# Optimization experiments

Measured on AMD Instinct MI355X. Metric: run time of the kernel, lower is better.

Reference implementation:

```python
import jax, jax.numpy as jnp
import numpy as np

NUM_EMBEDDINGS = 1024
EMBEDDING_DIM = 256
COMMITMENT_COST = 0.25


def setup_inputs() -> dict:
    key = jax.random.key(0)
    k1, k2 = jax.random.split(key)
    inputs = jax.random.normal(k1, (64, 32, 32, EMBEDDING_DIM), dtype=jnp.float32)
    embed = jax.random.normal(k2, (NUM_EMBEDDINGS, EMBEDDING_DIM), dtype=jnp.float32)
    return {"inputs": inputs, "embed": embed}


def reference(inputs, embed):
    # Eval-mode forward (no EMA buffer mutation), use_ema=True loss branch.
    input_shape = inputs.shape
    flat = inputs.reshape(-1, EMBEDDING_DIM)  # [N, d]
    distances = (
        jnp.sum(flat * flat, axis=1, keepdims=True)
        + jnp.sum(embed * embed, axis=1)
        - 2.0 * jnp.matmul(flat, embed.T)
    )
    encoding_indices = jnp.argmin(distances, axis=1)  # [N]
    # Gather codebook rows (equivalent to one-hot @ embed)
    quantized = embed[encoding_indices].reshape(input_shape)
    # use_ema branch: loss = commitment * mse(stop_grad(quantized), inputs)
    e_latent_loss = jnp.mean((jax.lax.stop_gradient(quantized) - inputs) ** 2)
    loss = COMMITMENT_COST * e_latent_loss
    # Straight-through estimator
    quantized_st = inputs + jax.lax.stop_gradient(quantized - inputs)
    # Perplexity from code usage histogram (== mean of one-hot encodings)
    n_tokens = flat.shape[0]
    counts = jax.ops.segment_sum(
        jnp.ones((n_tokens,), dtype=jnp.float32), encoding_indices,
        num_segments=NUM_EMBEDDINGS)
    avg_probs = counts / n_tokens
    perplexity = jnp.exp(-jnp.sum(avg_probs * jnp.log(avg_probs + 1e-10)))
    return quantized_st, loss, perplexity, encoding_indices
```

## Files before the change

kernel.cpp:

```cpp
#include <hip/hip_runtime.h>

#define NTOK 65536
#define DIM 256
#define KC 1024
#define EPS 0.08f

typedef __attribute__((ext_vector_type(8))) _Float16 f16x8;
typedef __attribute__((ext_vector_type(8))) unsigned short u16x8;
typedef __attribute__((ext_vector_type(4))) float f32x4;

static __device__ __forceinline__ unsigned short f16bits(float f) {
  _Float16 h = (_Float16)f;
  return __builtin_bit_cast(unsigned short, h);
}

__global__ __launch_bounds__(256) void vq_prep_e(const float* __restrict__ e,
                                                 unsigned short* __restrict__ eg,
                                                 float* __restrict__ esq,
                                                 int* __restrict__ hist,
                                                 int* __restrict__ fixCount) {
  const int gid = blockIdx.x * 256 + threadIdx.x;
  const int t = gid >> 5;
  const int o = gid & 31;
  const float4 v0 = *reinterpret_cast<const float4*>(&e[t * DIM + o * 8]);
  const float4 v1 = *reinterpret_cast<const float4*>(&e[t * DIM + o * 8 + 4]);
  u16x8 u;
  u[0] = f16bits(v0.x); u[1] = f16bits(v0.y); u[2] = f16bits(v0.z); u[3] = f16bits(v0.w);
  u[4] = f16bits(v1.x); u[5] = f16bits(v1.y); u[6] = f16bits(v1.z); u[7] = f16bits(v1.w);
  const int ct = t >> 7, nj = (t >> 4) & 7, col = t & 15;
  const int s = o >> 2, kq = o & 3;
  char* dst = (char*)eg + ((ct * 64 + s * 8 + nj) << 10) + ((kq * 16 + col) << 4);
  *reinterpret_cast<u16x8*>(dst) = u;
  float p = v0.x * v0.x + v0.y * v0.y + v0.z * v0.z + v0.w * v0.w +
            v1.x * v1.x + v1.y * v1.y + v1.z * v1.z + v1.w * v1.w;
#pragma unroll
  for (int m = 16; m > 0; m >>= 1) p += __shfl_xor(p, m, 64);
  if (o == 0) esq[t] = p;
  if (blockIdx.x < 4) hist[blockIdx.x * 256 + threadIdx.x] = 0;
  if (gid == 0) *fixCount = 0;
}

__global__ __launch_bounds__(64, 4) void vq_argmin(
    const float* __restrict__ x, const unsigned short* __restrict__ eg,
    const float* __restrict__ esq, const float* __restrict__ e,
    float* __restrict__ outIdxF, float* __restrict__ outQ,
    float* __restrict__ bestDist, float* __restrict__ xsq,
    int* __restrict__ hist, int* __restrict__ fixCount,
    unsigned int* __restrict__ fixList) {
  const int lane = threadIdx.x;
  const int col = lane & 15, kq = lane >> 4;
  const int tw = blockIdx.x * 16;

  f16x8 a[8];
  float sq = 0.f;
#pragma unroll
  for (int s = 0; s < 8; ++s) {
    const float* xp = &x[(tw + col) * DIM + s * 32 + kq * 8];
    const float4 v0 = *reinterpret_cast<const float4*>(xp);
    const float4 v1 = *reinterpret_cast<const float4*>(xp + 4);
    a[s][0] = (_Float16)v0.x; a[s][1] = (_Float16)v0.y;
    a[s][2] = (_Float16)v0.z; a[s][3] = (_Float16)v0.w;
    a[s][4] = (_Float16)v1.x; a[s][5] = (_Float16)v1.y;
    a[s][6] = (_Float16)v1.z; a[s][7] = (_Float16)v1.w;
    sq += v0.x * v0.x + v0.y * v0.y + v0.z * v0.z + v0.w * v0.w +
          v1.x * v1.x + v1.y * v1.y + v1.z * v1.z + v1.w * v1.w;
  }
  sq += __shfl_xor(sq, 16, 64);
  sq += __shfl_xor(sq, 32, 64);
  if (lane < 16) xsq[tw + lane] = sq;

  float v1_[4], v2_[4], v3_[4];
  int i1_[4], i2_[4];
#pragma unroll
  for (int r = 0; r < 4; ++r) {
    v1_[r] = 3.4e38f; v2_[r] = 3.4e38f; v3_[r] = 3.4e38f;
    i1_[r] = 0; i2_[r] = 0;
  }

  for (int ct = 0; ct < 8; ++ct) {
    const char* ebase = (const char*)eg + ct * 65536;
    f32x4 acc[8];
#pragma unroll
    for (int nj = 0; nj < 8; ++nj) acc[nj] = (f32x4){0.f, 0.f, 0.f, 0.f};

#pragma unroll
    for (int s = 0; s < 8; ++s) {
      f16x8 b[8];
#pragma unroll
      for (int nj = 0; nj < 8; ++nj)
        b[nj] = *reinterpret_cast<const f16x8*>(
            ebase + ((s * 8 + nj) << 10) + (lane << 4));
#pragma unroll
      for (int nj = 0; nj < 8; ++nj)
        acc[nj] = __builtin_amdgcn_mfma_f32_16x16x32_f16(a[s], b[nj], acc[nj], 0, 0, 0);
    }

#pragma unroll
    for (int nj = 0; nj < 8; ++nj) {
      const int code = ct * 128 + nj * 16 + col;
      const float sqv = esq[code];
#pragma unroll
      for (int r = 0; r < 4; ++r) {
        const float d = fmaf(-2.f, acc[nj][r], sqv);
        if (d < v1_[r]) {
          v3_[r] = v2_[r]; v2_[r] = v1_[r]; i2_[r] = i1_[r];
          v1_[r] = d; i1_[r] = code;
        } else if (d < v2_[r]) {
          v3_[r] = v2_[r]; v2_[r] = d; i2_[r] = code;
        } else if (d < v3_[r]) {
          v3_[r] = d;
        }
      }
    }
  }

#pragma unroll
  for (int r = 0; r < 4; ++r) {
    float mv1 = v1_[r], mv2 = v2_[r], mv3 = v3_[r];
    int mi1 = i1_[r], mi2 = i2_[r];
#pragma unroll
    for (int m = 1; m <= 8; m <<= 1) {
      const float ov1 = __shfl_xor(mv1, m, 64);
      const float ov2 = __shfl_xor(mv2, m, 64);
      const float ov3 = __shfl_xor(mv3, m, 64);
      const int oi1 = __shfl_xor(mi1, m, 64);
      const int oi2 = __shfl_xor(mi2, m, 64);
      const bool oW = (ov1 < mv1) || (ov1 == mv1 && oi1 < mi1);
      const float wv1 = oW ? ov1 : mv1, wv2 = oW ? ov2 : mv2, wv3 = oW ? ov3 : mv3;
      const int wi1 = oW ? oi1 : mi1, wi2 = oW ? oi2 : mi2;
      const float lv1 = oW ? mv1 : ov1, lv2 = oW ? mv2 : ov2;
      const int li1 = oW ? mi1 : oi1;
      const bool w2 = (wv2 < lv1) || (wv2 == lv1 && wi2 < li1);
      mv1 = wv1; mi1 = wi1;
      mv2 = w2 ? wv2 : lv1;
      mi2 = w2 ? wi2 : li1;
      mv3 = w2 ? fminf(wv3, lv1) : fminf(wv2, lv2);
    }
    if (col == 0) {
      const int t = tw + kq * 4 + r;
      outIdxF[t] = (float)mi1;
      bestDist[t] = mv1;
      atomicAdd(&hist[mi1], 1);
      if (mv2 - mv1 < EPS) {
        const unsigned full = (mv3 - mv1 < EPS) ? 0x80000000u : 0u;
        const int p = atomicAdd(fixCount, 1);
        fixList[p * 2] = (unsigned)t | full;
        fixList[p * 2 + 1] = (unsigned)mi2;
      }
    }
    i1_[r] = mi1;
  }

#pragma unroll
  for (int i = 0; i < 16; ++i) {
    const int id = __shfl(i1_[i & 3], (i >> 2) * 16, 64);
    const float4 q = reinterpret_cast<const float4*>(&e[id * DIM])[lane];
    reinterpret_cast<float4*>(&outQ[(tw + i) * DIM])[lane] = q;
  }
}

__global__ __launch_bounds__(256) void vq_fixup(
    const float* __restrict__ x, const float* __restrict__ e,
    const int* __restrict__ fixCount, const unsigned int* __restrict__ fixList,
    float* __restrict__ outIdxF, float* __restrict__ outQ,
    float* __restrict__ bestDist, int* __restrict__ hist) {
  const int n = *fixCount;
  const int tid = threadIdx.x;
  __shared__ float xrow[256];
  __shared__ float rv[4];
  __shared__ int ri[4];
  __shared__ int sOld, sFi;
  for (int it = blockIdx.x; it < n; it += gridDim.x) {
    const unsigned e0 = fixList[it * 2];
    const int t = (int)(e0 & 0x3FFFFFFFu);
    const bool full = (e0 >> 31) != 0u;
    if (!full) {
      if (tid < 64) {
        const int i1 = (int)outIdxF[t];
        const int i2 = (int)fixList[it * 2 + 1];
        const float4 xv = reinterpret_cast<const float4*>(&x[t * DIM])[tid];
        const float4 e1 = reinterpret_cast<const float4*>(&e[i1 * DIM])[tid];
        const float4 e2 = reinterpret_cast<const float4*>(&e[i2 * DIM])[tid];
        float d1 = (xv.x - e1.x) * (xv.x - e1.x) + (xv.y - e1.y) * (xv.y - e1.y) +
                   (xv.z - e1.z) * (xv.z - e1.z) + (xv.w - e1.w) * (xv.w - e1.w);
        float d2 = (xv.x - e2.x) * (xv.x - e2.x) + (xv.y - e2.y) * (xv.y - e2.y) +
                   (xv.z - e2.z) * (xv.z - e2.z) + (xv.w - e2.w) * (xv.w - e2.w);
#pragma unroll
        for (int m = 32; m > 0; m >>= 1) {
          d1 += __shfl_xor(d1, m, 64);
          d2 += __shfl_xor(d2, m, 64);
        }
        const bool swap2 = (d2 < d1) || (d2 == d1 && i2 < i1);
        const int wIdx = swap2 ? i2 : i1;
        const float wD = swap2 ? d2 : d1;
        if (tid == 0) {
          bestDist[t] = wD;
          if (wIdx != i1) {
            atomicSub(&hist[i1], 1);
            atomicAdd(&hist[wIdx], 1);
            outIdxF[t] = (float)wIdx;
          }
        }
        if (swap2) {
          const float4 q = reinterpret_cast<const float4*>(&e[wIdx * DIM])[tid];
          reinterpret_cast<float4*>(&outQ[t * DIM])[tid] = q;
        }
      }
    } else {
      __syncthreads();
      if (tid < 64) ((float4*)xrow)[tid] = ((const float4*)&x[t * DIM])[tid];
      __syncthreads();
      float bv = 3.4e38f; int bi = 0;
      for (int c = tid; c < KC; c += 256) {
        float s = 0.f;
#pragma unroll
        for (int d = 0; d < DIM; d += 4) {
          const float4 ev = *(const float4*)&e[c * DIM + d];
          const float d0 = xrow[d] - ev.x, d1 = xrow[d + 1] - ev.y;
          const float d2 = xrow[d + 2] - ev.z, d3 = xrow[d + 3] - ev.w;
          s += d0 * d0 + d1 * d1 + d2 * d2 + d3 * d3;
        }
        if (s < bv) { bv = s; bi = c; }
      }
#pragma unroll
      for (int m = 1; m <= 32; m <<= 1) {
        const float ob = __shfl_xor(bv, m, 64);
        const int oi = __shfl_xor(bi, m, 64);
        if (ob < bv || (ob == bv && oi < bi)) { bv = ob; bi = oi; }
      }
      const int lane = tid & 63, wv = tid >> 6;
      if (lane == 0) { rv[wv] = bv; ri[wv] = bi; }
      __syncthreads();
      if (tid == 0) {
        float fb = rv[0]; int fi = ri[0];
        for (int k = 1; k < 4; ++k)
          if (rv[k] < fb || (rv[k] == fb && ri[k] < fi)) { fb = rv[k]; fi = ri[k]; }
        sOld = (int)outIdxF[t];
        sFi = fi;
        bestDist[t] = fb;
        if (fi != sOld) {
          atomicSub(&hist[sOld], 1);
          atomicAdd(&hist[fi], 1);
          outIdxF[t] = (float)fi;
        }
      }
      __syncthreads();
      if (sFi != sOld) outQ[t * DIM + tid] = e[sFi * DIM + tid];
      __syncthreads();
    }
  }
}

__global__ __launch_bounds__(1024) void vq_final(
    const int* __restrict__ hist, const float* __restrict__ xsq,
    const float* __restrict__ bestDist, float* __restrict__ outLoss,
    float* __restrict__ outPerp) {
  const int tid = threadIdx.x;
  float ls = 0.f;
  for (int i = 0; i < 64; ++i) {
    const int t = tid + i * 1024;
    ls += xsq[t] + bestDist[t];
  }
  const float p = (float)hist[tid] * (1.f / 65536.f);
  float ent = p * logf(p + 1e-10f);
#pragma unroll
  for (int o = 32; o > 0; o >>= 1) {
    ls += __shfl_down(ls, o, 64);
    ent += __shfl_down(ent, o, 64);
  }
  __shared__ float lbuf[16], ebuf[16];
  const int lane = tid & 63, wv = tid >> 6;
  if (lane == 0) { lbuf[wv] = ls; ebuf[wv] = ent; }
  __syncthreads();
  if (tid == 0) {
    float L = 0.f, E = 0.f;
    for (int i = 0; i < 16; ++i) { L += lbuf[i]; E += ebuf[i]; }
    *outLoss = 0.25f * (L / 16777216.f);
    *outPerp = expf(-E);
  }
}

extern "C" void kernel_launch(void* const* d_in, const int* in_sizes, int n_in,
                              void* d_out, int out_size, void* d_ws, size_t ws_size,
                              hipStream_t stream) {
  const float* x = (const float*)d_in[0];
  const float* e = (const float*)d_in[1];
  float* out = (float*)d_out;
  float* outQ = out;
  float* outLoss = out + 16777216;
  float* outPerp = out + 16777217;
  float* outIdxF = out + 16777218;

  char* ws = (char*)d_ws;
  int*   hist     = (int*)ws;
  float* esq      = (float*)(ws + 4096);
  float* xsq      = (float*)(ws + 8192);
  float* bestDist = (float*)(ws + 270336);
  int*   fixCount = (int*)(ws + 532480);
  unsigned int* fixList = (unsigned int*)(ws + 532496);
  unsigned short* e_f16 = (unsigned short*)(ws + 1056784);

  vq_prep_e<<<128, 256, 0, stream>>>(e, e_f16, esq, hist, fixCount);
  vq_argmin<<<NTOK / 16, 64, 0, stream>>>(x, e_f16, esq, e, outIdxF, outQ,
                                          bestDist, xsq, hist, fixCount, fixList);
  vq_fixup<<<256, 256, 0, stream>>>(x, e, fixCount, fixList, outIdxF, outQ,
                                    bestDist, hist);
  vq_final<<<1, 1024, 0, stream>>>(hist, xsq, bestDist, outLoss, outPerp);
}
```

Measured before the change: 189.8 us.

## Double-buffer codebook fragment loads and pack four waves per argmin block

The argmin kernel now software-pipelines the f16 codebook loads with two register buffers, so the next k-slice, including the first slice of the next code tile, is fetched while MFMAs run on the current one. Blocks grow from one wave to four waves covering 64 tokens, with launch bounds changed to 256 threads and 3 blocks per CU. The aim is to hide global/L2 load latency behind matrix work. In exchange it doubles the B-fragment register footprint, which may push register use up and lower occupancy.

```diff
diff --git a/kernel.cpp b/kernel.cpp
--- a/kernel.cpp
+++ b/kernel.cpp
@@ -40,16 +40,16 @@
   if (gid == 0) *fixCount = 0;
 }
 
-__global__ __launch_bounds__(64, 4) void vq_argmin(
+__global__ __launch_bounds__(256, 3) void vq_argmin(
     const float* __restrict__ x, const unsigned short* __restrict__ eg,
     const float* __restrict__ esq, const float* __restrict__ e,
     float* __restrict__ outIdxF, float* __restrict__ outQ,
     float* __restrict__ bestDist, float* __restrict__ xsq,
     int* __restrict__ hist, int* __restrict__ fixCount,
     unsigned int* __restrict__ fixList) {
-  const int lane = threadIdx.x;
+  const int lane = threadIdx.x & 63, w = threadIdx.x >> 6;
   const int col = lane & 15, kq = lane >> 4;
-  const int tw = blockIdx.x * 16;
+  const int tw = blockIdx.x * 64 + w * 16;
 
   f16x8 a[8];
   float sq = 0.f;
@@ -69,6 +69,18 @@
   sq += __shfl_xor(sq, 32, 64);
   if (lane < 16) xsq[tw + lane] = sq;
 
+  auto LD8 = [&](f16x8 (&buf)[8], const char* eb, int s) {
+#pragma unroll
+    for (int nj = 0; nj < 8; ++nj)
+      buf[nj] = *reinterpret_cast<const f16x8*>(
+          eb + ((s * 8 + nj) << 10) + (lane << 4));
+  };
+  auto MF8 = [&](const f16x8& av, f16x8 (&buf)[8], f32x4 (&acc)[8]) {
+#pragma unroll
+    for (int nj = 0; nj < 8; ++nj)
+      acc[nj] = __builtin_amdgcn_mfma_f32_16x16x32_f16(av, buf[nj], acc[nj], 0, 0, 0);
+  };
+
   float v1_[4], v2_[4], v3_[4];
   int i1_[4], i2_[4];
 #pragma unroll
@@ -77,23 +89,24 @@
     i1_[r] = 0; i2_[r] = 0;
   }
 
+  f16x8 bA[8], bB[8];
+  LD8(bA, (const char*)eg, 0);
+
   for (int ct = 0; ct < 8; ++ct) {
-    const char* ebase = (const char*)eg + ct * 65536;
+    const char* eb = (const char*)eg + ct * 65536;
     f32x4 acc[8];
 #pragma unroll
     for (int nj = 0; nj < 8; ++nj) acc[nj] = (f32x4){0.f, 0.f, 0.f, 0.f};
 
-#pragma unroll
-    for (int s = 0; s < 8; ++s) {
-      f16x8 b[8];
-#pragma unroll
-      for (int nj = 0; nj < 8; ++nj)
-        b[nj] = *reinterpret_cast<const f16x8*>(
-            ebase + ((s * 8 + nj) << 10) + (lane << 4));
-#pragma unroll
-      for (int nj = 0; nj < 8; ++nj)
-        acc[nj] = __builtin_amdgcn_mfma_f32_16x16x32_f16(a[s], b[nj], acc[nj], 0, 0, 0);
-    }
+    LD8(bB, eb, 1); MF8(a[0], bA, acc);
+    LD8(bA, eb, 2); MF8(a[1], bB, acc);
+    LD8(bB, eb, 3); MF8(a[2], bA, acc);
+    LD8(bA, eb, 4); MF8(a[3], bB, acc);
+    LD8(bB, eb, 5); MF8(a[4], bA, acc);
+    LD8(bA, eb, 6); MF8(a[5], bB, acc);
+    LD8(bB, eb, 7); MF8(a[6], bA, acc);
+    if (ct < 7) LD8(bA, eb + 65536, 0);
+    MF8(a[7], bB, acc);
 
 #pragma unroll
     for (int nj = 0; nj < 8; ++nj) {
@@ -301,8 +314,8 @@
   unsigned short* e_f16 = (unsigned short*)(ws + 1056784);
 
   vq_prep_e<<<128, 256, 0, stream>>>(e, e_f16, esq, hist, fixCount);
-  vq_argmin<<<NTOK / 16, 64, 0, stream>>>(x, e_f16, esq, e, outIdxF, outQ,
-                                          bestDist, xsq, hist, fixCount, fixList);
+  vq_argmin<<<NTOK / 64, 256, 0, stream>>>(x, e_f16, esq, e, outIdxF, outQ,
+                                           bestDist, xsq, hist, fixCount, fixList);
   vq_fixup<<<256, 256, 0, stream>>>(x, e, fixCount, fixList, outIdxF, outQ,
                                     bestDist, hist);
   vq_final<<<1, 1024, 0, stream>>>(hist, xsq, bestDist, outLoss, outPerp);
```

Result: slower. 208.9 us (+10.0%).

## Pipeline codebook loads with inline asm and double tokens per wave

Applied to the files above, without the earlier changes.

Each wave now handles 32 tokens (two 16-row A tiles) instead of 16, so every codebook fragment loaded feeds twice as many MFMAs, and blocks grow to four waves. The codebook layout is regrouped into 64-code chunks, streamed through a four-stage register ring with inline-asm global loads and explicit vmcnt waits plus sched barriers, so loads overlap the MFMAs. This targets codebook load bandwidth and exposed latency, at the cost of higher register pressure (two waves per SIMD bound) and fragile hand-counted waitcnt logic.

```diff
diff --git a/kernel.cpp b/kernel.cpp
--- a/kernel.cpp
+++ b/kernel.cpp
@@ -13,6 +13,12 @@
   _Float16 h = (_Float16)f;
   return __builtin_bit_cast(unsigned short, h);
 }
+
+#define VWAIT(n) asm volatile("s_waitcnt vmcnt(" #n ")" ::: "memory")
+#define SB() __builtin_amdgcn_sched_barrier(0)
+#define GLDX4(dst, p, off) \
+  asm volatile("global_load_dwordx4 %0, %1, off offset:" #off \
+               : "=v"(dst) : "v"(p) : "memory")
 
 __global__ __launch_bounds__(256) void vq_prep_e(const float* __restrict__ e,
                                                  unsigned short* __restrict__ eg,
@@ -27,9 +33,9 @@
   u16x8 u;
   u[0] = f16bits(v0.x); u[1] = f16bits(v0.y); u[2] = f16bits(v0.z); u[3] = f16bits(v0.w);
   u[4] = f16bits(v1.x); u[5] = f16bits(v1.y); u[6] = f16bits(v1.z); u[7] = f16bits(v1.w);
-  const int ct = t >> 7, nj = (t >> 4) & 7, col = t & 15;
+  const int ctk = t >> 6, njj = (t >> 4) & 3, col = t & 15;
   const int s = o >> 2, kq = o & 3;
-  char* dst = (char*)eg + ((ct * 64 + s * 8 + nj) << 10) + ((kq * 16 + col) << 4);
+  char* dst = (char*)eg + ((ctk * 32 + s * 4 + njj) << 10) + ((kq * 16 + col) << 4);
   *reinterpret_cast<u16x8*>(dst) = u;
   float p = v0.x * v0.x + v0.y * v0.y + v0.z * v0.z + v0.w * v0.w +
             v1.x * v1.x + v1.y * v1.y + v1.z * v1.z + v1.w * v1.w;
@@ -40,120 +46,185 @@
   if (gid == 0) *fixCount = 0;
 }
 
-__global__ __launch_bounds__(64, 4) void vq_argmin(
+__global__ __launch_bounds__(256, 2) void vq_argmin(
     const float* __restrict__ x, const unsigned short* __restrict__ eg,
     const float* __restrict__ esq, const float* __restrict__ e,
     float* __restrict__ outIdxF, float* __restrict__ outQ,
     float* __restrict__ bestDist, float* __restrict__ xsq,
     int* __restrict__ hist, int* __restrict__ fixCount,
     unsigned int* __restrict__ fixList) {
-  const int lane = threadIdx.x;
+  const int lane = threadIdx.x & 63, w = threadIdx.x >> 6;
   const int col = lane & 15, kq = lane >> 4;
-  const int tw = blockIdx.x * 16;
-
-  f16x8 a[8];
-  float sq = 0.f;
-#pragma unroll
-  for (int s = 0; s < 8; ++s) {
-    const float* xp = &x[(tw + col) * DIM + s * 32 + kq * 8];
-    const float4 v0 = *reinterpret_cast<const float4*>(xp);
-    const float4 v1 = *reinterpret_cast<const float4*>(xp + 4);
-    a[s][0] = (_Float16)v0.x; a[s][1] = (_Float16)v0.y;
-    a[s][2] = (_Float16)v0.z; a[s][3] = (_Float16)v0.w;
-    a[s][4] = (_Float16)v1.x; a[s][5] = (_Float16)v1.y;
-    a[s][6] = (_Float16)v1.z; a[s][7] = (_Float16)v1.w;
-    sq += v0.x * v0.x + v0.y * v0.y + v0.z * v0.z + v0.w * v0.w +
-          v1.x * v1.x + v1.y * v1.y + v1.z * v1.z + v1.w * v1.w;
-  }
-  sq += __shfl_xor(sq, 16, 64);
-  sq += __shfl_xor(sq, 32, 64);
-  if (lane < 16) xsq[tw + lane] = sq;
-
-  float v1_[4], v2_[4], v3_[4];
-  int i1_[4], i2_[4];
-#pragma unroll
-  for (int r = 0; r < 4; ++r) {
-    v1_[r] = 3.4e38f; v2_[r] = 3.4e38f; v3_[r] = 3.4e38f;
-    i1_[r] = 0; i2_[r] = 0;
-  }
-
-  for (int ct = 0; ct < 8; ++ct) {
-    const char* ebase = (const char*)eg + ct * 65536;
-    f32x4 acc[8];
-#pragma unroll
-    for (int nj = 0; nj < 8; ++nj) acc[nj] = (f32x4){0.f, 0.f, 0.f, 0.f};
-
+  const int tw = blockIdx.x * 128 + w * 32;
+
+  f16x8 a[2][8];
+  float sqm[2] = {0.f, 0.f};
+#pragma unroll
+  for (int mi = 0; mi < 2; ++mi) {
 #pragma unroll
     for (int s = 0; s < 8; ++s) {
-      f16x8 b[8];
-#pragma unroll
-      for (int nj = 0; nj < 8; ++nj)
-        b[nj] = *reinterpret_cast<const f16x8*>(
-            ebase + ((s * 8 + nj) << 10) + (lane << 4));
-#pragma unroll
-      for (int nj = 0; nj < 8; ++nj)
-        acc[nj] = __builtin_amdgcn_mfma_f32_16x16x32_f16(a[s], b[nj], acc[nj], 0, 0, 0);
-    }
-
-#pragma unroll
-    for (int nj = 0; nj < 8; ++nj) {
-      const int code = ct * 128 + nj * 16 + col;
-      const float sqv = esq[code];
-#pragma unroll
-      for (int r = 0; r < 4; ++r) {
-        const float d = fmaf(-2.f, acc[nj][r], sqv);
-        if (d < v1_[r]) {
-          v3_[r] = v2_[r]; v2_[r] = v1_[r]; i2_[r] = i1_[r];
-          v1_[r] = d; i1_[r] = code;
-        } else if (d < v2_[r]) {
-          v3_[r] = v2_[r]; v2_[r] = d; i2_[r] = code;
-        } else if (d < v3_[r]) {
-          v3_[r] = d;
-        }
-      }
-    }
-  }
-
-#pragma unroll
-  for (int r = 0; r < 4; ++r) {
-    float mv1 = v1_[r], mv2 = v2_[r], mv3 = v3_[r];
-    int mi1 = i1_[r], mi2 = i2_[r];
-#pragma unroll
-    for (int m = 1; m <= 8; m <<= 1) {
-      const float ov1 = __shfl_xor(mv1, m, 64);
-      const float ov2 = __shfl_xor(mv2, m, 64);
-      const float ov3 = __shfl_xor(mv3, m, 64);
-      const int oi1 = __shfl_xor(mi1, m, 64);
-      const int oi2 = __shfl_xor(mi2, m, 64);
-      const bool oW = (ov1 < mv1) || (ov1 == mv1 && oi1 < mi1);
-      const float wv1 = oW ? ov1 : mv1, wv2 = oW ? ov2 : mv2, wv3 = oW ? ov3 : mv3;
-      const int wi1 = oW ? oi1 : mi1, wi2 = oW ? oi2 : mi2;
-      const float lv1 = oW ? mv1 : ov1, lv2 = oW ? mv2 : ov2;
-      const int li1 = oW ? mi1 : oi1;
-      const bool w2 = (wv2 < lv1) || (wv2 == lv1 && wi2 < li1);
-      mv1 = wv1; mi1 = wi1;
-      mv2 = w2 ? wv2 : lv1;
-      mi2 = w2 ? wi2 : li1;
-      mv3 = w2 ? fminf(wv3, lv1) : fminf(wv2, lv2);
-    }
-    if (col == 0) {
-      const int t = tw + kq * 4 + r;
-      outIdxF[t] = (float)mi1;
-      bestDist[t] = mv1;
-      atomicAdd(&hist[mi1], 1);
-      if (mv2 - mv1 < EPS) {
-        const unsigned full = (mv3 - mv1 < EPS) ? 0x80000000u : 0u;
-        const int p = atomicAdd(fixCount, 1);
-        fixList[p * 2] = (unsigned)t | full;
-        fixList[p * 2 + 1] = (unsigned)mi2;
-      }
-    }
-    i1_[r] = mi1;
-  }
-
-#pragma unroll
-  for (int i = 0; i < 16; ++i) {
-    const int id = __shfl(i1_[i & 3], (i >> 2) * 16, 64);
+      const float* xp = &x[(tw + mi * 16 + col) * DIM + s * 32 + kq * 8];
+      const float4 v0 = *reinterpret_cast<const float4*>(xp);
+      const float4 v1 = *reinterpret_cast<const float4*>(xp + 4);
+      a[mi][s][0] = (_Float16)v0.x; a[mi][s][1] = (_Float16)v0.y;
+      a[mi][s][2] = (_Float16)v0.z; a[mi][s][3] = (_Float16)v0.w;
+      a[mi][s][4] = (_Float16)v1.x; a[mi][s][5] = (_Float16)v1.y;
+      a[mi][s][6] = (_Float16)v1.z; a[mi][s][7] = (_Float16)v1.w;
+      sqm[mi] += v0.x * v0.x + v0.y * v0.y + v0.z * v0.z + v0.w * v0.w +
+                 v1.x * v1.x + v1.y * v1.y + v1.z * v1.z + v1.w * v1.w;
+    }
+  }
+#pragma unroll
+  for (int mi = 0; mi < 2; ++mi) {
+    sqm[mi] += __shfl_xor(sqm[mi], 16, 64);
+    sqm[mi] += __shfl_xor(sqm[mi], 32, 64);
+  }
+  if (lane < 16) {
+    xsq[tw + lane] = sqm[0];
+    xsq[tw + 16 + lane] = sqm[1];
+  }
+
+  float v1_[2][4], v2_[2][4], v3_[2][4];
+  int i1_[2][4], i2_[2][4];
+#pragma unroll
+  for (int mi = 0; mi < 2; ++mi)
+#pragma unroll
+    for (int r = 0; r < 4; ++r) {
+      v1_[mi][r] = 3.4e38f; v2_[mi][r] = 3.4e38f; v3_[mi][r] = 3.4e38f;
+      i1_[mi][r] = 0; i2_[mi][r] = 0;
+    }
+
+  f32x4 acc[2][4];
+  f16x8 B[4][4];
+  const char* p = (const char*)eg + lane * 16;
+
+  VWAIT(0);
+  SB();
+#pragma unroll
+  for (int g = 0; g < 4; ++g) {
+    GLDX4(B[g][0], p, 0); GLDX4(B[g][1], p, 1024);
+    GLDX4(B[g][2], p, 2048); GLDX4(B[g][3], p, 3072);
+    p += 4096;
+  }
+
+#define STEP_BODY(S, BUF)                                                     \
+  do {                                                                        \
+    acc[0][0] = __builtin_amdgcn_mfma_f32_16x16x32_f16(a[0][(S)], BUF[0], acc[0][0], 0, 0, 0); \
+    acc[0][1] = __builtin_amdgcn_mfma_f32_16x16x32_f16(a[0][(S)], BUF[1], acc[0][1], 0, 0, 0); \
+    acc[0][2] = __builtin_amdgcn_mfma_f32_16x16x32_f16(a[0][(S)], BUF[2], acc[0][2], 0, 0, 0); \
+    acc[0][3] = __builtin_amdgcn_mfma_f32_16x16x32_f16(a[0][(S)], BUF[3], acc[0][3], 0, 0, 0); \
+    acc[1][0] = __builtin_amdgcn_mfma_f32_16x16x32_f16(a[1][(S)], BUF[0], acc[1][0], 0, 0, 0); \
+    acc[1][1] = __builtin_amdgcn_mfma_f32_16x16x32_f16(a[1][(S)], BUF[1], acc[1][1], 0, 0, 0); \
+    acc[1][2] = __builtin_amdgcn_mfma_f32_16x16x32_f16(a[1][(S)], BUF[2], acc[1][2], 0, 0, 0); \
+    acc[1][3] = __builtin_amdgcn_mfma_f32_16x16x32_f16(a[1][(S)], BUF[3], acc[1][3], 0, 0, 0); \
+  } while (0)
+
+#define ISSUE(BUF)                                                 \
+  do {                                                             \
+    GLDX4(BUF[0], p, 0); GLDX4(BUF[1], p, 1024);                   \
+    GLDX4(BUF[2], p, 2048); GLDX4(BUF[3], p, 3072);                \
+    p += 4096;                                                     \
+  } while (0)
+
+#define EPILOGUE(CTK)                                                         \
+  do {                                                                        \
+    const float* pe = &esq[(CTK) * 64 + col];                                 \
+    _Pragma("unroll") for (int njj = 0; njj < 4; ++njj) {                     \
+      const int code = (CTK) * 64 + njj * 16 + col;                           \
+      const float sqv = pe[njj * 16];                                         \
+      _Pragma("unroll") for (int mi = 0; mi < 2; ++mi)                        \
+      _Pragma("unroll") for (int r = 0; r < 4; ++r) {                         \
+        const float d = fmaf(-2.f, acc[mi][njj][r], sqv);                     \
+        if (d < v1_[mi][r]) {                                                 \
+          v3_[mi][r] = v2_[mi][r]; v2_[mi][r] = v1_[mi][r];                   \
+          i2_[mi][r] = i1_[mi][r];                                            \
+          v1_[mi][r] = d; i1_[mi][r] = code;                                  \
+        } else if (d < v2_[mi][r]) {                                          \
+          v3_[mi][r] = v2_[mi][r]; v2_[mi][r] = d; i2_[mi][r] = code;         \
+        } else if (d < v3_[mi][r]) {                                          \
+          v3_[mi][r] = d;                                                     \
+        }                                                                     \
+      }                                                                       \
+    }                                                                         \
+  } while (0)
+
+  for (int ctk = 0; ctk < 15; ++ctk) {
+#pragma unroll
+    for (int mi = 0; mi < 2; ++mi)
+#pragma unroll
+      for (int nj = 0; nj < 4; ++nj) acc[mi][nj] = (f32x4){0.f, 0.f, 0.f, 0.f};
+#pragma unroll
+    for (int s = 0; s < 8; ++s) {
+      VWAIT(12);
+      SB();
+      if ((s & 3) == 0) { STEP_BODY(s, B[0]); ISSUE(B[0]); }
+      else if ((s & 3) == 1) { STEP_BODY(s, B[1]); ISSUE(B[1]); }
+      else if ((s & 3) == 2) { STEP_BODY(s, B[2]); ISSUE(B[2]); }
+      else { STEP_BODY(s, B[3]); ISSUE(B[3]); }
+    }
+    EPILOGUE(ctk);
+  }
+  {
+#pragma unroll
+    for (int mi = 0; mi < 2; ++mi)
+#pragma unroll
+      for (int nj = 0; nj < 4; ++nj) acc[mi][nj] = (f32x4){0.f, 0.f, 0.f, 0.f};
+    VWAIT(12); SB(); STEP_BODY(0, B[0]); ISSUE(B[0]);
+    VWAIT(12); SB(); STEP_BODY(1, B[1]); ISSUE(B[1]);
+    VWAIT(12); SB(); STEP_BODY(2, B[2]); ISSUE(B[2]);
+    VWAIT(12); SB(); STEP_BODY(3, B[3]); ISSUE(B[3]);
+    VWAIT(12); SB(); STEP_BODY(4, B[0]);
+    VWAIT(8);  SB(); STEP_BODY(5, B[1]);
+    VWAIT(4);  SB(); STEP_BODY(6, B[2]);
+    VWAIT(0);  SB(); STEP_BODY(7, B[3]);
+    EPILOGUE(15);
+  }
+#undef STEP_BODY
+#undef ISSUE
+#undef EPILOGUE
+
+#pragma unroll
+  for (int mi = 0; mi < 2; ++mi)
+#pragma unroll
+    for (int r = 0; r < 4; ++r) {
+      float mv1 = v1_[mi][r], mv2 = v2_[mi][r], mv3 = v3_[mi][r];
+      int mi1 = i1_[mi][r], mi2 = i2_[mi][r];
+#pragma unroll
+      for (int m = 1; m <= 8; m <<= 1) {
+        const float ov1 = __shfl_xor(mv1, m, 64);
+        const float ov2 = __shfl_xor(mv2, m, 64);
+        const float ov3 = __shfl_xor(mv3, m, 64);
+        const int oi1 = __shfl_xor(mi1, m, 64);
+        const int oi2 = __shfl_xor(mi2, m, 64);
+        const bool oW = (ov1 < mv1) || (ov1 == mv1 && oi1 < mi1);
+        const float wv1 = oW ? ov1 : mv1, wv2 = oW ? ov2 : mv2, wv3 = oW ? ov3 : mv3;
+        const int wi1 = oW ? oi1 : mi1, wi2 = oW ? oi2 : mi2;
+        const float lv1 = oW ? mv1 : ov1, lv2 = oW ? mv2 : ov2;
+        const int li1 = oW ? mi1 : oi1;
+        const bool w2 = (wv2 < lv1) || (wv2 == lv1 && wi2 < li1);
+        mv1 = wv1; mi1 = wi1;
+        mv2 = w2 ? wv2 : lv1;
+        mi2 = w2 ? wi2 : li1;
+        mv3 = w2 ? fminf(wv3, lv1) : fminf(wv2, lv2);
+      }
+      if (col == 0) {
+        const int t = tw + mi * 16 + kq * 4 + r;
+        outIdxF[t] = (float)mi1;
+        bestDist[t] = mv1;
+        atomicAdd(&hist[mi1], 1);
+        if (mv2 - mv1 < EPS) {
+          const unsigned full = (mv3 - mv1 < EPS) ? 0x80000000u : 0u;
+          const int pp = atomicAdd(fixCount, 1);
+          fixList[pp * 2] = (unsigned)t | full;
+          fixList[pp * 2 + 1] = (unsigned)mi2;
+        }
+      }
+      i1_[mi][r] = mi1;
+    }
+
+#pragma unroll
+  for (int i = 0; i < 32; ++i) {
+    const int id = __shfl(i1_[i >> 4][i & 3], ((i >> 2) & 3) * 16, 64);
     const float4 q = reinterpret_cast<const float4*>(&e[id * DIM])[lane];
     reinterpret_cast<float4*>(&outQ[(tw + i) * DIM])[lane] = q;
   }
@@ -301,8 +372,8 @@
   unsigned short* e_f16 = (unsigned short*)(ws + 1056784);
 
   vq_prep_e<<<128, 256, 0, stream>>>(e, e_f16, esq, hist, fixCount);
-  vq_argmin<<<NTOK / 16, 64, 0, stream>>>(x, e_f16, esq, e, outIdxF, outQ,
-                                          bestDist, xsq, hist, fixCount, fixList);
+  vq_argmin<<<NTOK / 128, 256, 0, stream>>>(x, e_f16, esq, e, outIdxF, outQ,
+                                            bestDist, xsq, hist, fixCount, fixList);
   vq_fixup<<<256, 256, 0, stream>>>(x, e, fixCount, fixList, outIdxF, outQ,
                                     bestDist, hist);
   vq_final<<<1, 1024, 0, stream>>>(hist, xsq, bestDist, outLoss, outPerp);
```

After: 164.9 us. -13.2%, faster.

## Swap MFMA operand roles: keep codebook slices in registers, stream pre-converted tokens

Applied to the files above, without the earlier changes.

Adds a prep kernel that converts inputs to f16 in an MFMA-friendly tiled layout and computes row norms. The argmin kernel now holds a 32-code slice of the codebook in registers per wave and streams token tiles through it. Each code partition writes per-token top-2 partial results to scratch space carved from the output buffer. A new finish kernel reduces the 32 partials per token and builds the fixup list, and a separate gather kernel writes the quantized rows. This removes the repeated full-codebook reload per 16-token wave, at the cost of extra kernels and roughly 1 GB of extra global traffic for the f16 copy and partial results, plus more atomics.

```diff
diff --git a/kernel.cpp b/kernel.cpp
--- a/kernel.cpp
+++ b/kernel.cpp
@@ -27,9 +27,9 @@
   u16x8 u;
   u[0] = f16bits(v0.x); u[1] = f16bits(v0.y); u[2] = f16bits(v0.z); u[3] = f16bits(v0.w);
   u[4] = f16bits(v1.x); u[5] = f16bits(v1.y); u[6] = f16bits(v1.z); u[7] = f16bits(v1.w);
-  const int ct = t >> 7, nj = (t >> 4) & 7, col = t & 15;
+  const int ctk = t >> 6, njj = (t >> 4) & 3, col = t & 15;
   const int s = o >> 2, kq = o & 3;
-  char* dst = (char*)eg + ((ct * 64 + s * 8 + nj) << 10) + ((kq * 16 + col) << 4);
+  char* dst = (char*)eg + ((ctk * 32 + s * 4 + njj) << 10) + ((kq * 16 + col) << 4);
   *reinterpret_cast<u16x8*>(dst) = u;
   float p = v0.x * v0.x + v0.y * v0.y + v0.z * v0.z + v0.w * v0.w +
             v1.x * v1.x + v1.y * v1.y + v1.z * v1.z + v1.w * v1.w;
@@ -40,122 +40,158 @@
   if (gid == 0) *fixCount = 0;
 }
 
-__global__ __launch_bounds__(64, 4) void vq_argmin(
-    const float* __restrict__ x, const unsigned short* __restrict__ eg,
-    const float* __restrict__ esq, const float* __restrict__ e,
-    float* __restrict__ outIdxF, float* __restrict__ outQ,
-    float* __restrict__ bestDist, float* __restrict__ xsq,
-    int* __restrict__ hist, int* __restrict__ fixCount,
-    unsigned int* __restrict__ fixList) {
-  const int lane = threadIdx.x;
+__global__ __launch_bounds__(256) void vq_prep_x(const float* __restrict__ x,
+                                                 unsigned short* __restrict__ xg,
+                                                 float* __restrict__ xsq) {
+  const int gid = blockIdx.x * 256 + threadIdx.x;
+  const int t = gid >> 5;
+  const int o = gid & 31;
+  const float4 v0 = *reinterpret_cast<const float4*>(&x[t * DIM + o * 8]);
+  const float4 v1 = *reinterpret_cast<const float4*>(&x[t * DIM + o * 8 + 4]);
+  u16x8 u;
+  u[0] = f16bits(v0.x); u[1] = f16bits(v0.y); u[2] = f16bits(v0.z); u[3] = f16bits(v0.w);
+  u[4] = f16bits(v1.x); u[5] = f16bits(v1.y); u[6] = f16bits(v1.z); u[7] = f16bits(v1.w);
+  const int s = o >> 2, kq = o & 3;
+  char* dst = (char*)xg + (((t >> 4) * 8 + s) << 10) + ((kq * 16 + (t & 15)) << 4);
+  *reinterpret_cast<u16x8*>(dst) = u;
+  float p = v0.x * v0.x + v0.y * v0.y + v0.z * v0.z + v0.w * v0.w +
+            v1.x * v1.x + v1.y * v1.y + v1.z * v1.z + v1.w * v1.w;
+#pragma unroll
+  for (int m = 16; m > 0; m >>= 1) p += __shfl_xor(p, m, 64);
+  if (o == 0) xsq[t] = p;
+}
+
+__global__ __launch_bounds__(256, 3) void vq_argmin(
+    const unsigned short* __restrict__ xg, const unsigned short* __restrict__ eg,
+    const float* __restrict__ esq, float* __restrict__ rV1,
+    unsigned int* __restrict__ rI1, float* __restrict__ rV2,
+    unsigned int* __restrict__ rI2) {
+  const int lane = threadIdx.x & 63, w = threadIdx.x >> 6;
   const int col = lane & 15, kq = lane >> 4;
-  const int tw = blockIdx.x * 16;
-
-  f16x8 a[8];
-  float sq = 0.f;
-#pragma unroll
-  for (int s = 0; s < 8; ++s) {
-    const float* xp = &x[(tw + col) * DIM + s * 32 + kq * 8];
-    const float4 v0 = *reinterpret_cast<const float4*>(xp);
-    const float4 v1 = *reinterpret_cast<const float4*>(xp + 4);
-    a[s][0] = (_Float16)v0.x; a[s][1] = (_Float16)v0.y;
-    a[s][2] = (_Float16)v0.z; a[s][3] = (_Float16)v0.w;
-    a[s][4] = (_Float16)v1.x; a[s][5] = (_Float16)v1.y;
-    a[s][6] = (_Float16)v1.z; a[s][7] = (_Float16)v1.w;
-    sq += v0.x * v0.x + v0.y * v0.y + v0.z * v0.z + v0.w * v0.w +
-          v1.x * v1.x + v1.y * v1.y + v1.z * v1.z + v1.w * v1.w;
-  }
-  sq += __shfl_xor(sq, 16, 64);
-  sq += __shfl_xor(sq, 32, 64);
-  if (lane < 16) xsq[tw + lane] = sq;
-
-  float v1_[4], v2_[4], v3_[4];
-  int i1_[4], i2_[4];
-#pragma unroll
-  for (int r = 0; r < 4; ++r) {
-    v1_[r] = 3.4e38f; v2_[r] = 3.4e38f; v3_[r] = 3.4e38f;
-    i1_[r] = 0; i2_[r] = 0;
-  }
-
-  for (int ct = 0; ct < 8; ++ct) {
-    const char* ebase = (const char*)eg + ct * 65536;
-    f32x4 acc[8];
-#pragma unroll
-    for (int nj = 0; nj < 8; ++nj) acc[nj] = (f32x4){0.f, 0.f, 0.f, 0.f};
-
+  const int cp = blockIdx.x & 7, tb = blockIdx.x >> 3;
+  const int cbase = cp * 128 + w * 32;
+  const int ctk = cbase >> 6;
+  const int njb = (w & 1) * 2;
+  const int pw = cp * 4 + w;
+
+  f16x8 ae[8][2];
+#pragma unroll
+  for (int s = 0; s < 8; ++s)
+#pragma unroll
+    for (int cg = 0; cg < 2; ++cg)
+      ae[s][cg] = *reinterpret_cast<const f16x8*>(
+          (const char*)eg + ((ctk * 32 + s * 4 + njb + cg) << 10) + (lane << 4));
+  float esr[2][4];
+#pragma unroll
+  for (int cg = 0; cg < 2; ++cg)
+#pragma unroll
+    for (int r = 0; r < 4; ++r)
+      esr[cg][r] = esq[cbase + cg * 16 + kq * 4 + r];
+
+  for (int i = 0; i < 16; ++i) {
+    const int tsub = tb * 16 + i;
+    f32x4 acc[2];
+    acc[0] = (f32x4){0.f, 0.f, 0.f, 0.f};
+    acc[1] = (f32x4){0.f, 0.f, 0.f, 0.f};
 #pragma unroll
     for (int s = 0; s < 8; ++s) {
-      f16x8 b[8];
-#pragma unroll
-      for (int nj = 0; nj < 8; ++nj)
-        b[nj] = *reinterpret_cast<const f16x8*>(
-            ebase + ((s * 8 + nj) << 10) + (lane << 4));
-#pragma unroll
-      for (int nj = 0; nj < 8; ++nj)
-        acc[nj] = __builtin_amdgcn_mfma_f32_16x16x32_f16(a[s], b[nj], acc[nj], 0, 0, 0);
+      const f16x8 bx = *reinterpret_cast<const f16x8*>(
+          (const char*)xg + ((tsub * 8 + s) << 10) + (lane << 4));
+      acc[0] = __builtin_amdgcn_mfma_f32_16x16x32_f16(ae[s][0], bx, acc[0], 0, 0, 0);
+      acc[1] = __builtin_amdgcn_mfma_f32_16x16x32_f16(ae[s][1], bx, acc[1], 0, 0, 0);
     }
-
-#pragma unroll
-    for (int nj = 0; nj < 8; ++nj) {
-      const int code = ct * 128 + nj * 16 + col;
-      const float sqv = esq[code];
+    float v1 = 3.4e38f, v2 = 3.4e38f, v3 = 3.4e38f;
+    int i1 = 0, i2 = 0;
+#pragma unroll
+    for (int cg = 0; cg < 2; ++cg)
 #pragma unroll
       for (int r = 0; r < 4; ++r) {
-        const float d = fmaf(-2.f, acc[nj][r], sqv);
-        if (d < v1_[r]) {
-          v3_[r] = v2_[r]; v2_[r] = v1_[r]; i2_[r] = i1_[r];
-          v1_[r] = d; i1_[r] = code;
-        } else if (d < v2_[r]) {
-          v3_[r] = v2_[r]; v2_[r] = d; i2_[r] = code;
-        } else if (d < v3_[r]) {
-          v3_[r] = d;
-        }
-      }
+        const int code = cbase + cg * 16 + kq * 4 + r;
+        const float d = fmaf(-2.f, acc[cg][r], esr[cg][r]);
+        if (d < v1) { v3 = v2; v2 = v1; i2 = i1; v1 = d; i1 = code; }
+        else if (d < v2) { v3 = v2; v2 = d; i2 = code; }
+        else if (d < v3) { v3 = d; }
+      }
+#pragma unroll
+    for (int m = 16; m <= 32; m <<= 1) {
+      const float ov1 = __shfl_xor(v1, m, 64);
+      const float ov2 = __shfl_xor(v2, m, 64);
+      const float ov3 = __shfl_xor(v3, m, 64);
+      const int oi1 = __shfl_xor(i1, m, 64);
+      const int oi2 = __shfl_xor(i2, m, 64);
+      const bool oW = (ov1 < v1) || (ov1 == v1 && oi1 < i1);
+      const float wv1 = oW ? ov1 : v1, wv2 = oW ? ov2 : v2, wv3 = oW ? ov3 : v3;
+      const int wi1 = oW ? oi1 : i1, wi2 = oW ? oi2 : i2;
+      const float lv1 = oW ? v1 : ov1, lv2 = oW ? v2 : ov2;
+      const int li1 = oW ? i1 : oi1;
+      const bool w2 = (wv2 < lv1) || (wv2 == lv1 && wi2 < li1);
+      v1 = wv1; i1 = wi1;
+      v2 = w2 ? wv2 : lv1;
+      i2 = w2 ? wi2 : li1;
+      v3 = w2 ? fminf(wv3, lv1) : fminf(wv2, lv2);
     }
-  }
-
-#pragma unroll
-  for (int r = 0; r < 4; ++r) {
-    float mv1 = v1_[r], mv2 = v2_[r], mv3 = v3_[r];
-    int mi1 = i1_[r], mi2 = i2_[r];
-#pragma unroll
-    for (int m = 1; m <= 8; m <<= 1) {
-      const float ov1 = __shfl_xor(mv1, m, 64);
-      const float ov2 = __shfl_xor(mv2, m, 64);
-      const float ov3 = __shfl_xor(mv3, m, 64);
-      const int oi1 = __shfl_xor(mi1, m, 64);
-      const int oi2 = __shfl_xor(mi2, m, 64);
-      const bool oW = (ov1 < mv1) || (ov1 == mv1 && oi1 < mi1);
-      const float wv1 = oW ? ov1 : mv1, wv2 = oW ? ov2 : mv2, wv3 = oW ? ov3 : mv3;
-      const int wi1 = oW ? oi1 : mi1, wi2 = oW ? oi2 : mi2;
-      const float lv1 = oW ? mv1 : ov1, lv2 = oW ? mv2 : ov2;
-      const int li1 = oW ? mi1 : oi1;
-      const bool w2 = (wv2 < lv1) || (wv2 == lv1 && wi2 < li1);
-      mv1 = wv1; mi1 = wi1;
-      mv2 = w2 ? wv2 : lv1;
-      mi2 = w2 ? wi2 : li1;
-      mv3 = w2 ? fminf(wv3, lv1) : fminf(wv2, lv2);
+    if (kq == 0) {
+      const int rb = pw * NTOK + tsub * 16 + col;
+      rV1[rb] = v1;
+      rI1[rb] = (unsigned)i1 | ((v3 - v1 < EPS) ? 0x80000000u : 0u);
+      rV2[rb] = v2;
+      rI2[rb] = (unsigned)i2;
     }
-    if (col == 0) {
-      const int t = tw + kq * 4 + r;
-      outIdxF[t] = (float)mi1;
-      bestDist[t] = mv1;
-      atomicAdd(&hist[mi1], 1);
-      if (mv2 - mv1 < EPS) {
-        const unsigned full = (mv3 - mv1 < EPS) ? 0x80000000u : 0u;
-        const int p = atomicAdd(fixCount, 1);
-        fixList[p * 2] = (unsigned)t | full;
-        fixList[p * 2 + 1] = (unsigned)mi2;
-      }
-    }
-    i1_[r] = mi1;
-  }
-
+  }
+}
+
+__global__ __launch_bounds__(256) void vq_finish1(
+    const float* __restrict__ rV1, const unsigned int* __restrict__ rI1,
+    const float* __restrict__ rV2, const unsigned int* __restrict__ rI2,
+    const float* __restrict__ xsq, float* __restrict__ outIdxF,
+    float* __restrict__ bestDist, int* __restrict__ hist,
+    int* __restrict__ fixCount, unsigned int* __restrict__ fixList) {
+  const int t = blockIdx.x * 256 + threadIdx.x;
+  float m1 = 3.4e38f, m2 = 3.4e38f, m3 = 3.4e38f;
+  int mi1 = 0x7FFFFFFF, mi2 = 0x7FFFFFFF;
+  float minFlagV1 = 3.4e38f;
+#pragma unroll
+  for (int p = 0; p < 32; ++p) {
+    const int rb = p * NTOK + t;
+    const float a1 = rV1[rb];
+    const unsigned u1 = rI1[rb];
+    const float a2 = rV2[rb];
+    const int ai2 = (int)rI2[rb];
+    const int ai1 = (int)(u1 & 0x7FFFFFFFu);
+    if (u1 >> 31) minFlagV1 = fminf(minFlagV1, a1);
+    if (a1 < m1 || (a1 == m1 && ai1 < mi1)) {
+      m3 = m2; m2 = m1; mi2 = mi1; m1 = a1; mi1 = ai1;
+    } else if (a1 < m2 || (a1 == m2 && ai1 < mi2)) {
+      m3 = m2; m2 = a1; mi2 = ai1;
+    } else if (a1 < m3) m3 = a1;
+    if (a2 < m1 || (a2 == m1 && ai2 < mi1)) {
+      m3 = m2; m2 = m1; mi2 = mi1; m1 = a2; mi1 = ai2;
+    } else if (a2 < m2 || (a2 == m2 && ai2 < mi2)) {
+      m3 = m2; m2 = a2; mi2 = ai2;
+    } else if (a2 < m3) m3 = a2;
+  }
+  outIdxF[t] = (float)mi1;
+  bestDist[t] = xsq[t] + m1;
+  atomicAdd(&hist[mi1], 1);
+  if (m2 - m1 < EPS) {
+    const bool full = (m3 - m1 < EPS) || (minFlagV1 - m1 < EPS);
+    const int p = atomicAdd(fixCount, 1);
+    fixList[p * 2] = (unsigned)t | (full ? 0x80000000u : 0u);
+    fixList[p * 2 + 1] = (unsigned)(mi2 & 0x3FF);
+  }
+}
+
+__global__ __launch_bounds__(256) void vq_gather(
+    const float* __restrict__ e, const float* __restrict__ outIdxF,
+    float* __restrict__ outQ) {
+  const int lane = threadIdx.x & 63, w = threadIdx.x >> 6;
+  const int t0 = blockIdx.x * 64 + w * 16;
 #pragma unroll
   for (int i = 0; i < 16; ++i) {
-    const int id = __shfl(i1_[i & 3], (i >> 2) * 16, 64);
+    const int t = t0 + i;
+    const int id = (int)outIdxF[t];
     const float4 q = reinterpret_cast<const float4*>(&e[id * DIM])[lane];
-    reinterpret_cast<float4*>(&outQ[(tw + i) * DIM])[lane] = q;
+    reinterpret_cast<float4*>(&outQ[t * DIM])[lane] = q;
   }
 }
 
@@ -252,15 +288,11 @@
 }
 
 __global__ __launch_bounds__(1024) void vq_final(
-    const int* __restrict__ hist, const float* __restrict__ xsq,
-    const float* __restrict__ bestDist, float* __restrict__ outLoss,
-    float* __restrict__ outPerp) {
+    const int* __restrict__ hist, const float* __restrict__ bestDist,
+    float* __restrict__ outLoss, float* __restrict__ outPerp) {
   const int tid = threadIdx.x;
   float ls = 0.f;
-  for (int i = 0; i < 64; ++i) {
-    const int t = tid + i * 1024;
-    ls += xsq[t] + bestDist[t];
-  }
+  for (int i = 0; i < 64; ++i) ls += bestDist[tid + i * 1024];
   const float p = (float)hist[tid] * (1.f / 65536.f);
   float ent = p * logf(p + 1e-10f);
 #pragma unroll
@@ -291,6 +323,12 @@
   float* outPerp = out + 16777217;
   float* outIdxF = out + 16777218;
 
+  unsigned short* xg = (unsigned short*)d_out;
+  float* rV1 = out + 8388608;
+  unsigned int* rI1 = (unsigned int*)(out + 10485760);
+  float* rV2 = out + 12582912;
+  unsigned int* rI2 = (unsigned int*)(out + 14680064);
+
   char* ws = (char*)d_ws;
   int*   hist     = (int*)ws;
   float* esq      = (float*)(ws + 4096);
@@ -301,9 +339,12 @@
   unsigned short* e_f16 = (unsigned short*)(ws + 1056784);
 
   vq_prep_e<<<128, 256, 0, stream>>>(e, e_f16, esq, hist, fixCount);
-  vq_argmin<<<NTOK / 16, 64, 0, stream>>>(x, e_f16, esq, e, outIdxF, outQ,
-                                          bestDist, xsq, hist, fixCount, fixList);
+  vq_prep_x<<<8192, 256, 0, stream>>>(x, xg, xsq);
+  vq_argmin<<<2048, 256, 0, stream>>>(xg, e_f16, esq, rV1, rI1, rV2, rI2);
+  vq_finish1<<<256, 256, 0, stream>>>(rV1, rI1, rV2, rI2, xsq, outIdxF,
+                                      bestDist, hist, fixCount, fixList);
+  vq_gather<<<1024, 256, 0, stream>>>(e, outIdxF, outQ);
   vq_fixup<<<256, 256, 0, stream>>>(x, e, fixCount, fixList, outIdxF, outQ,
                                     bestDist, hist);
-  vq_final<<<1, 1024, 0, stream>>>(hist, xsq, bestDist, outLoss, outPerp);
-}
+  vq_final<<<1, 1024, 0, stream>>>(hist, bestDist, outLoss, outPerp);
+}
```

After: 200.5 us. 1.06x slower.
